# Kernel optimization log

Measured on AMD Instinct MI355X. Metric: run time of the kernel, lower is better.

The kernel has to match this reference:

```python
import jax, jax.numpy as jnp
import numpy as np

TAU = 2.0      # LIF membrane time constant
ALPHA = 4.0    # sigmoid surrogate sharpness (spikingjelly default)
EPS = 1e-5     # BatchNorm eps
HEADS = 8


def lif(x, vth):
    """MultiStepLIFNode: scan over leading time dim T. Hard reset to 0, detach_reset.
    Forward spike = heaviside(h - vth); backward uses sigmoid surrogate via straight-through."""
    def step(v, xt):
        h = v + (xt - v) / TAU
        hv = h - vth
        sg = jax.nn.sigmoid(ALPHA * hv)
        hard = (hv >= 0).astype(h.dtype)
        spike = sg + jax.lax.stop_gradient(hard - sg)
        v_new = h * (1.0 - jax.lax.stop_gradient(spike))  # detach_reset=True, v_reset=0
        return v_new, spike
    _, spikes = jax.lax.scan(step, jnp.zeros_like(x[0]), x)
    return spikes


def bn(x, gamma, beta, mean, var):
    # x: (T,B,C,N), params: (C,) ; eval-mode BatchNorm1d over channel axis 2
    inv = (gamma * jax.lax.rsqrt(var + EPS))[None, None, :, None]
    return (x - mean[None, None, :, None]) * inv + beta[None, None, :, None]


def setup_inputs() -> dict:
    key = jax.random.key(0)
    T, B, C, H, W = 4, 16, 384, 32, 32
    ks = jax.random.split(key, 24)
    d = {"x": jax.random.normal(ks[0], (T, B, C, H, W), jnp.float32)}
    i = 1
    wscale = 1.0 / np.sqrt(C)
    for p in ("q", "k", "v", "p"):
        d[p + "_w"] = jax.random.normal(ks[i], (C, C), jnp.float32) * wscale; i += 1
        d[p + "_gamma"] = jax.random.uniform(ks[i], (C,), jnp.float32, 0.5, 1.5); i += 1
        d[p + "_beta"] = jax.random.normal(ks[i], (C,), jnp.float32) * 0.1; i += 1
        d[p + "_mean"] = jax.random.normal(ks[i], (C,), jnp.float32) * 0.1; i += 1
        d[p + "_var"] = jax.random.uniform(ks[i], (C,), jnp.float32, 0.5, 1.5); i += 1
    d["p_bias"] = jax.random.normal(ks[i], (C,), jnp.float32) * 0.1
    return d


def reference(x, q_w, q_gamma, q_beta, q_mean, q_var,
              k_w, k_gamma, k_beta, k_mean, k_var,
              v_w, v_gamma, v_beta, v_mean, v_var,
              p_w, p_bias, p_gamma, p_beta, p_mean, p_var):
    T, B, C, H, W = x.shape
    N = H * W
    Ch = C // HEADS
    # input spiking (named proj_lif in source, applied first)
    xs = lif(x, 1.0).reshape(T, B, C, N)

    def branch(w, g, b, m, v):
        y = jnp.einsum('tbcn,dc->tbdn', xs, w)  # 1x1 Conv1d == channel matmul
        return lif(bn(y, g, b, m, v), 1.0).reshape(T, B, HEADS, Ch, N)

    q = branch(q_w, q_gamma, q_beta, q_mean, q_var)
    k = branch(k_w, k_gamma, k_beta, k_mean, k_var)
    v = branch(v_w, v_gamma, v_beta, v_mean, v_var)

    attn = jnp.sum(k * v, axis=3, keepdims=True)  # (T,B,h,1,N)
    attn = lif(attn, 0.5)
    out = (q * attn).reshape(T, B, C, N)
    out = jnp.einsum('tbcn,dc->tbdn', out, p_w) + p_bias[None, None, :, None]
    out = bn(out, p_gamma, p_beta, p_mean, p_var)
    return out.reshape(T, B, C, H, W)
```

## Files before the change

kernel.cpp:

```cpp
#include <hip/hip_runtime.h>

typedef unsigned short u16;
typedef unsigned char u8;
typedef unsigned int u32;
typedef float f32x4 __attribute__((ext_vector_type(4)));
typedef __bf16 bf16x8 __attribute__((ext_vector_type(8)));

#define SPB 6291456

__device__ __forceinline__ void gll16(const void* g, void* l) {
  __builtin_amdgcn_global_load_lds((const __attribute__((address_space(1))) void*)g,
                                   (__attribute__((address_space(3))) void*)l, 16, 0, 0);
}

__device__ __forceinline__ uint4 expand8(uint2 v, u32 t) {
  u32 a = v.x >> t, b = v.y >> t;
  uint4 r;
  r.x = ((a & 1u) ? 0x3F80u : 0u) | ((a & 0x100u) ? 0x3F800000u : 0u);
  r.y = ((a & 0x10000u) ? 0x3F80u : 0u) | ((a & 0x1000000u) ? 0x3F800000u : 0u);
  r.z = ((b & 1u) ? 0x3F80u : 0u) | ((b & 0x100u) ? 0x3F800000u : 0u);
  r.w = ((b & 0x10000u) ? 0x3F80u : 0u) | ((b & 0x1000000u) ? 0x3F800000u : 0u);
  return r;
}

__global__ __launch_bounds__(256) void k_convert(
    const float* __restrict__ qw, const float* __restrict__ kw,
    const float* __restrict__ vw, const float* __restrict__ pw,
    const float* __restrict__ qg, const float* __restrict__ qbt,
    const float* __restrict__ qm, const float* __restrict__ qv,
    const float* __restrict__ kg, const float* __restrict__ kbt,
    const float* __restrict__ km, const float* __restrict__ kv,
    const float* __restrict__ vg, const float* __restrict__ vbt,
    const float* __restrict__ vm, const float* __restrict__ vv,
    const float* __restrict__ pg, const float* __restrict__ pbt,
    const float* __restrict__ pm, const float* __restrict__ pv,
    const float* __restrict__ pbias,
    u16* __restrict__ Wstk, u16* __restrict__ Pw,
    float4* __restrict__ BNP, float4* __restrict__ PP) {
  int tid = blockIdx.x * 256 + threadIdx.x;
  if (tid < 442368) {
    int r = tid / 384, c = tid - r * 384;
    const float* src = (r < 384) ? qw : (r < 768) ? kw : vw;
    int rr = (r >= 768) ? r - 768 : (r >= 384) ? r - 384 : r;
    unsigned int u = __float_as_uint(src[rr * 384 + c]);
    u = (u + 0x7FFFu + ((u >> 16) & 1u)) >> 16;
    Wstk[tid] = (u16)u;
  } else if (tid < 589824) {
    int i = tid - 442368;
    unsigned int u = __float_as_uint(pw[i]);
    u = (u + 0x7FFFu + ((u >> 16) & 1u)) >> 16;
    Pw[i] = (u16)u;
  } else if (tid < 590976) {
    int r = tid - 589824;
    int br = r / 384, ch = r - br * 384;
    const float* g  = (br == 0) ? qg  : (br == 1) ? kg  : vg;
    const float* bt = (br == 0) ? qbt : (br == 1) ? kbt : vbt;
    const float* m  = (br == 0) ? qm  : (br == 1) ? km  : vm;
    const float* va = (br == 0) ? qv  : (br == 1) ? kv  : vv;
    float inv = g[ch] / sqrtf(va[ch] + 1e-5f);
    BNP[r] = make_float4(inv, m[ch], bt[ch], 0.f);
  } else if (tid < 591360) {
    int ch = tid - 590976;
    float inv = pg[ch] / sqrtf(pv[ch] + 1e-5f);
    PP[ch] = make_float4(inv, pm[ch], pbt[ch], pbias[ch]);
  }
}

__global__ __launch_bounds__(256) void k_lif_in(const float* __restrict__ x, u8* __restrict__ xsb) {
  const int nt = blockIdx.x, ct = blockIdx.y, b = blockIdx.z;
  const int tid = threadIdx.x;
  const int nj = tid & 63, cr = tid >> 6;
  const int c0 = ct * 64, n0 = nt * 64;
  __shared__ u32 nibs[64 * 65];
  float v[16];
  u32 nib[16];
  #pragma unroll
  for (int i = 0; i < 16; ++i) { v[i] = 0.f; nib[i] = 0u; }
  for (int t = 0; t < 4; ++t) {
    const float* xr = x + (((t * 16 + b) * 384 + c0 + cr) * 1024) + n0 + nj;
    #pragma unroll
    for (int it = 0; it < 16; ++it) {
      float xv = xr[it * 4096];
      float vv = v[it];
      float h = __fadd_rn(vv, __fmul_rn(__fsub_rn(xv, vv), 0.5f));
      bool s = h >= 1.f;
      v[it] = s ? 0.f : h;
      nib[it] |= (s ? 1u : 0u) << t;
    }
  }
  #pragma unroll
  for (int it = 0; it < 16; ++it) nibs[nj * 65 + cr + it * 4] = nib[it];
  __syncthreads();
  const int n = tid >> 2, ch = tid & 3;
  u32 w0[4];
  #pragma unroll
  for (int q = 0; q < 4; ++q) {
    u32 acc = 0;
    #pragma unroll
    for (int i = 0; i < 4; ++i)
      acc |= (nibs[n * 65 + ch * 16 + q * 4 + i] & 0xFu) << (8 * i);
    w0[q] = acc;
  }
  *(uint4*)(xsb + ((size_t)(b * 1024 + n0 + n)) * 384 + c0 + ch * 16) =
      make_uint4(w0[0], w0[1], w0[2], w0[3]);
}

#define GISSUE(kt) do { \
    gll16(Wp + (kt) * 32, &lds[((kt) % 3) * 12288 + wst]); \
    xr0[(kt) % 3] = *(const uint2*)(Xb0 + (kt) * 32); \
    xr1[(kt) % 3] = *(const uint2*)(Xb1 + (kt) * 32); \
  } while (0)

#define GWRITE(kt) do { \
    *(uint4*)&lds[((kt) % 3) * 12288 + 4096 + wst + lx8] = expand8(xr0[(kt) % 3], t_row); \
    *(uint4*)&lds[((kt) % 3) * 12288 + 8192 + wst + lx8] = expand8(xr1[(kt) % 3], t_row); \
  } while (0)

#define COMPUTE(bufi) do { \
    const u16* lb_ = &lds[(bufi) * 12288]; \
    bf16x8 ax[4], bw[4]; \
    _Pragma("unroll") \
    for (int ji = 0; ji < 4; ++ji) \
      ax[ji] = *(const bf16x8*)&lb_[4096 + (wjg * 64 + ji * 16 + l15) * 32 + swoff]; \
    _Pragma("unroll") \
    for (int ci = 0; ci < 4; ++ci) \
      bw[ci] = *(const bf16x8*)&lb_[(wcg * 64 + ci * 16 + l15) * 32 + swoff]; \
    __builtin_amdgcn_s_setprio(1); \
    _Pragma("unroll") \
    for (int ji = 0; ji < 4; ++ji) \
      _Pragma("unroll") \
      for (int ci = 0; ci < 4; ++ci) \
        acc[ji][ci] = __builtin_amdgcn_mfma_f32_16x16x32_bf16(ax[ji], bw[ci], acc[ji][ci], 0, 0, 0); \
    __builtin_amdgcn_s_setprio(0); \
  } while (0)

#define GSTEP(kt, VN, ISS) do { \
    asm volatile("s_waitcnt vmcnt(" #VN ")" ::: "memory"); \
    GWRITE(kt); \
    asm volatile("s_waitcnt lgkmcnt(0)" ::: "memory"); \
    __builtin_amdgcn_s_barrier(); \
    asm volatile("" ::: "memory"); \
    ISS; \
    COMPUTE((kt) % 3); \
  } while (0)

#define GEMM_PIPELINE() do { \
    GISSUE(0); GISSUE(1); \
    GSTEP(0, 3, GISSUE(2)); \
    GSTEP(1, 3, GISSUE(3)); \
    GSTEP(2, 3, GISSUE(4)); \
    GSTEP(3, 3, GISSUE(5)); \
    GSTEP(4, 3, GISSUE(6)); \
    GSTEP(5, 3, GISSUE(7)); \
    GSTEP(6, 3, GISSUE(8)); \
    GSTEP(7, 3, GISSUE(9)); \
    GSTEP(8, 3, GISSUE(10)); \
    GSTEP(9, 3, GISSUE(11)); \
    GSTEP(10, 3, ); \
    GSTEP(11, 0, ); \
  } while (0)

#define GEMM_SETUP(WSRC, XSRC) \
  const int tid = threadIdx.x; \
  const int w = tid >> 6, l = tid & 63; \
  const int wjg = w >> 1, wcg = w & 1; \
  const int l15 = tid & 15; \
  const int swoff = (((tid & 63) >> 4) ^ ((l15 >> 1) & 3)) * 8; \
  const int m0 = mt * 128; \
  const int wst = w * 512; \
  const int lx8 = l * 8; \
  const int row = w * 16 + (l >> 2); \
  const u32 t_row = (u32)(row & 3); \
  const int sch = (l & 3) ^ ((l >> 3) & 3); \
  const u16* Wp = (WSRC) + (m0 + row) * 384 + sch * 8; \
  const u8* Xb0 = (XSRC) + ((size_t)(b * 1024 + jt * 64 + (row >> 2))) * 384 + sch * 8; \
  const u8* Xb1 = Xb0 + 32 * 384; \
  uint2 xr0[3], xr1[3]; \
  f32x4 acc[4][4]; \
  const f32x4 zero = {0.f, 0.f, 0.f, 0.f}; \
  _Pragma("unroll") \
  for (int ji = 0; ji < 4; ++ji) \
    _Pragma("unroll") \
    for (int ci = 0; ci < 4; ++ci) acc[ji][ci] = zero;

__global__ __launch_bounds__(512, 4) void k_qkv(
    const u16* __restrict__ Wstk, const u8* __restrict__ xsb,
    const float4* __restrict__ BNP, u8* __restrict__ sp) {
  const int jt = blockIdx.x, mt = blockIdx.y, b = blockIdx.z;
  __shared__ u16 lds[36864];
  __shared__ float4 PRM[128];
  if (threadIdx.x < 128) PRM[threadIdx.x] = BNP[mt * 128 + threadIdx.x];
  __syncthreads();

  GEMM_SETUP(Wstk, xsb);
  GEMM_PIPELINE();

  const int br = mt / 3;
  const int cb = (mt - br * 3) * 128;
  const int g = (tid & 63) >> 4;
  u8* spW = sp + (size_t)br * SPB;
  #pragma unroll
  for (int ci = 0; ci < 4; ++ci) {
    const int c_loc = wcg * 64 + ci * 16 + l15;
    float4 pr = PRM[c_loc];
    #pragma unroll
    for (int ji = 0; ji < 4; ++ji) {
      f32x4 a = acc[ji][ci];
      u32 bits = 0;
      float v = 0.f;
      #pragma unroll
      for (int t = 0; t < 4; ++t) {
        float z = __fadd_rn(__fmul_rn(__fsub_rn(a[t], pr.y), pr.x), pr.z);
        float h = __fadd_rn(v, __fmul_rn(__fsub_rn(z, v), 0.5f));
        bool s = h >= 1.f;
        v = s ? 0.f : h;
        bits |= (s ? 1u : 0u) << t;
      }
      const int n_comb = b * 1024 + jt * 64 + wjg * 16 + ji * 4 + g;
      spW[(size_t)n_comb * 384 + cb + c_loc] = (u8)bits;
    }
  }
}

__global__ __launch_bounds__(256) void k_attn(const u8* __restrict__ sp, u8* __restrict__ xpb) {
  const int gw = blockIdx.x * 4 + (threadIdx.x >> 6);
  const int l = threadIdx.x & 63;
  const int b = gw >> 10, n = gw & 1023;
  const u8* qB = sp;
  const u8* kB = sp + SPB;
  const u8* vB = sp + 2 * SPB;
  const int base = (b * 1024 + n) * 384 + l * 6;
  u16 qu[3], ku[3], vu[3];
  #pragma unroll
  for (int i = 0; i < 3; ++i) {
    qu[i] = *(const u16*)(qB + base + 2 * i);
    ku[i] = *(const u16*)(kB + base + 2 * i);
    vu[i] = *(const u16*)(vB + base + 2 * i);
  }
  u32 s = 0;
  #pragma unroll
  for (int i = 0; i < 3; ++i) {
    u32 a = (u32)(ku[i] & vu[i]);
    #pragma unroll
    for (int t = 0; t < 4; ++t) {
      u32 x = (a >> t) & 0x0101u;
      s += ((x + (x >> 8)) & 3u) << (8 * t);
    }
  }
  s += __shfl_xor(s, 1);
  s += __shfl_xor(s, 2);
  s += __shfl_xor(s, 4);
  float v = 0.f;
  u32 m8 = 0;
  #pragma unroll
  for (int t = 0; t < 4; ++t) {
    float attn = (float)((s >> (8 * t)) & 0xFFu);
    float h = __fadd_rn(v, __fmul_rn(__fsub_rn(attn, v), 0.5f));
    bool sk = h >= 0.5f;
    v = sk ? 0.f : h;
    m8 |= (sk ? 1u : 0u) << t;
  }
  const u16 mm = (u16)(m8 * 0x0101u);
  u16* dst = (u16*)(xpb + base);
  #pragma unroll
  for (int i = 0; i < 3; ++i) dst[i] = qu[i] & mm;
}

__global__ __launch_bounds__(512, 4) void k_proj(
    const u16* __restrict__ Pw, const u8* __restrict__ xpb,
    const float4* __restrict__ PP, float* __restrict__ out) {
  const int jt = blockIdx.x, mt = blockIdx.y, b = blockIdx.z;
  __shared__ u16 lds[36864];
  __shared__ float4 PRM[128];
  if (threadIdx.x < 128) PRM[threadIdx.x] = PP[mt * 128 + threadIdx.x];
  __syncthreads();

  GEMM_SETUP(Pw, xpb);
  GEMM_PIPELINE();

  __syncthreads();
  float* scr = (float*)lds;
  const int n0im = jt * 64;
  const int g = (tid & 63) >> 4;

  #pragma unroll
  for (int t = 0; t < 4; ++t) {
    #pragma unroll
    for (int ci = 0; ci < 4; ++ci) {
      const int c_loc = wcg * 64 + ci * 16 + l15;
      float4 pr = PRM[c_loc];
      #pragma unroll
      for (int ji = 0; ji < 4; ++ji) {
        const int n_loc = wjg * 16 + ji * 4 + g;
        float zz = __fadd_rn(acc[ji][ci][t], pr.w);
        zz = __fadd_rn(__fmul_rn(__fsub_rn(zz, pr.y), pr.x), pr.z);
        scr[c_loc * 68 + n_loc] = zz;
      }
    }
    __syncthreads();
    #pragma unroll
    for (int it = 0; it < 4; ++it) {
      int slot = tid + it * 512;
      int c = slot >> 4, li = slot & 15;
      float4 val = *(const float4*)&scr[c * 68 + li * 4];
      *(float4*)&out[(((size_t)(t * 16 + b) * 384) + mt * 128 + c) * 1024 + n0im + li * 4] = val;
    }
    __syncthreads();
  }
}

extern "C" void kernel_launch(void* const* d_in, const int* in_sizes, int n_in,
                              void* d_out, int out_size, void* d_ws, size_t ws_size,
                              hipStream_t stream) {
  (void)in_sizes; (void)n_in; (void)out_size; (void)ws_size;
  const float* x   = (const float*)d_in[0];
  const float* qw  = (const float*)d_in[1];
  const float* qg  = (const float*)d_in[2];
  const float* qbt = (const float*)d_in[3];
  const float* qm  = (const float*)d_in[4];
  const float* qv  = (const float*)d_in[5];
  const float* kw  = (const float*)d_in[6];
  const float* kg  = (const float*)d_in[7];
  const float* kbt = (const float*)d_in[8];
  const float* km  = (const float*)d_in[9];
  const float* kv  = (const float*)d_in[10];
  const float* vw  = (const float*)d_in[11];
  const float* vg  = (const float*)d_in[12];
  const float* vbt = (const float*)d_in[13];
  const float* vm  = (const float*)d_in[14];
  const float* vv  = (const float*)d_in[15];
  const float* pw  = (const float*)d_in[16];
  const float* pg  = (const float*)d_in[17];
  const float* pbt = (const float*)d_in[18];
  const float* pm  = (const float*)d_in[19];
  const float* pv  = (const float*)d_in[20];
  const float* pbias = (const float*)d_in[21];

  char* ws = (char*)d_ws;
  u8*  xsb   = (u8*)ws;
  u8*  sp    = (u8*)(ws + 6291456);
  u8*  xpb   = (u8*)(ws + 25165824);
  u16* Wstk  = (u16*)(ws + 31457280);
  u16* Pw    = (u16*)(ws + 32342016);
  float4* BNP = (float4*)(ws + 32636928);
  float4* PP  = (float4*)(ws + 32655360);

  k_convert<<<2310, 256, 0, stream>>>(qw, kw, vw, pw, qg, qbt, qm, qv, kg, kbt, km, kv,
                                      vg, vbt, vm, vv, pg, pbt, pm, pv, pbias,
                                      Wstk, Pw, BNP, PP);
  k_lif_in<<<dim3(16, 6, 16), 256, 0, stream>>>(x, xsb);
  k_qkv<<<dim3(16, 9, 16), 512, 0, stream>>>(Wstk, xsb, BNP, sp);
  k_attn<<<4096, 256, 0, stream>>>(sp, xpb);
  k_proj<<<dim3(16, 3, 16), 512, 0, stream>>>(Pw, xpb, PP, (float*)d_out);
}
```

Measured before the change: 130.3 us.

## Compute three weight tiles per block to reuse expanded spike tiles in GEMMs

Each GEMM block now loads and expands its spike activation tile once, then multiplies it against three 128-row weight tiles (the q/k/v branches in qkv, all three output-channel slices in proj) with three accumulator sets. This cuts redundant activation loads and bit-to-bf16 expansion, and the grids shrink by a factor of three. The spike expansion also switches to byte-permute and multiply instead of per-bit selects. In exchange, register use and LDS per block grow (occupancy hint drops from 4 to 2), and proj now launches only 256 blocks, which may underfill the GPU.

```diff
diff --git a/kernel.cpp b/kernel.cpp
--- a/kernel.cpp
+++ b/kernel.cpp
@@ -13,13 +13,14 @@
                                    (__attribute__((address_space(3))) void*)l, 16, 0, 0);
 }
 
-__device__ __forceinline__ uint4 expand8(uint2 v, u32 t) {
-  u32 a = v.x >> t, b = v.y >> t;
+__device__ __forceinline__ uint4 expand8f(uint2 v, u32 t) {
+  u32 a = (v.x >> t) & 0x01010101u;
+  u32 b = (v.y >> t) & 0x01010101u;
   uint4 r;
-  r.x = ((a & 1u) ? 0x3F80u : 0u) | ((a & 0x100u) ? 0x3F800000u : 0u);
-  r.y = ((a & 0x10000u) ? 0x3F80u : 0u) | ((a & 0x1000000u) ? 0x3F800000u : 0u);
-  r.z = ((b & 1u) ? 0x3F80u : 0u) | ((b & 0x100u) ? 0x3F800000u : 0u);
-  r.w = ((b & 0x10000u) ? 0x3F80u : 0u) | ((b & 0x1000000u) ? 0x3F800000u : 0u);
+  r.x = __builtin_amdgcn_perm(0u, a, 0x0C010C00u) * 0x3F80u;
+  r.y = __builtin_amdgcn_perm(0u, a, 0x0C030C02u) * 0x3F80u;
+  r.z = __builtin_amdgcn_perm(0u, b, 0x0C010C00u) * 0x3F80u;
+  r.w = __builtin_amdgcn_perm(0u, b, 0x0C030C02u) * 0x3F80u;
   return r;
 }
 
@@ -105,121 +106,135 @@
       make_uint4(w0[0], w0[1], w0[2], w0[3]);
 }
 
+#define BUFU16 20480
+
 #define GISSUE(kt) do { \
-    gll16(Wp + (kt) * 32, &lds[((kt) % 3) * 12288 + wst]); \
+    u16* wb_ = &lds[((kt) % 3) * BUFU16 + wst]; \
+    gll16(Wp0 + (kt) * 32, wb_); \
+    gll16(Wp1 + (kt) * 32, wb_ + 4096); \
+    gll16(Wp2 + (kt) * 32, wb_ + 8192); \
     xr0[(kt) % 3] = *(const uint2*)(Xb0 + (kt) * 32); \
     xr1[(kt) % 3] = *(const uint2*)(Xb1 + (kt) * 32); \
   } while (0)
 
 #define GWRITE(kt) do { \
-    *(uint4*)&lds[((kt) % 3) * 12288 + 4096 + wst + lx8] = expand8(xr0[(kt) % 3], t_row); \
-    *(uint4*)&lds[((kt) % 3) * 12288 + 8192 + wst + lx8] = expand8(xr1[(kt) % 3], t_row); \
-  } while (0)
-
-#define COMPUTE(bufi) do { \
-    const u16* lb_ = &lds[(bufi) * 12288]; \
-    bf16x8 ax[4], bw[4]; \
+    *(uint4*)&lds[((kt) % 3) * BUFU16 + 12288 + tid * 8] = expand8f(xr0[(kt) % 3], t_row); \
+    *(uint4*)&lds[((kt) % 3) * BUFU16 + 12288 + 4096 + tid * 8] = expand8f(xr1[(kt) % 3], t_row); \
+  } while (0)
+
+#define MFMA4(accA, p) do { \
+    _Pragma("unroll") \
+    for (int ci = 0; ci < 4; ++ci) { \
+      bf16x8 bw_ = *(const bf16x8*)&lb_[(p) * 4096 + (wcg * 64 + ci * 16 + l15) * 32 + swoff]; \
+      _Pragma("unroll") \
+      for (int ji = 0; ji < 4; ++ji) \
+        accA[ji][ci] = __builtin_amdgcn_mfma_f32_16x16x32_bf16(ax[ji], bw_, accA[ji][ci], 0, 0, 0); \
+    } \
+  } while (0)
+
+#define COMPUTE3(bufi) do { \
+    const u16* lb_ = &lds[(bufi) * BUFU16]; \
+    bf16x8 ax[4]; \
     _Pragma("unroll") \
     for (int ji = 0; ji < 4; ++ji) \
-      ax[ji] = *(const bf16x8*)&lb_[4096 + (wjg * 64 + ji * 16 + l15) * 32 + swoff]; \
-    _Pragma("unroll") \
-    for (int ci = 0; ci < 4; ++ci) \
-      bw[ci] = *(const bf16x8*)&lb_[(wcg * 64 + ci * 16 + l15) * 32 + swoff]; \
+      ax[ji] = *(const bf16x8*)&lb_[12288 + (wjg * 64 + ji * 16 + l15) * 32 + swoff]; \
     __builtin_amdgcn_s_setprio(1); \
-    _Pragma("unroll") \
-    for (int ji = 0; ji < 4; ++ji) \
-      _Pragma("unroll") \
-      for (int ci = 0; ci < 4; ++ci) \
-        acc[ji][ci] = __builtin_amdgcn_mfma_f32_16x16x32_bf16(ax[ji], bw[ci], acc[ji][ci], 0, 0, 0); \
+    MFMA4(acc0, 0); MFMA4(acc1, 1); MFMA4(acc2, 2); \
     __builtin_amdgcn_s_setprio(0); \
   } while (0)
 
-#define GSTEP(kt, VN, ISS) do { \
+#define GSTEP(t, VN, TAIL) do { \
     asm volatile("s_waitcnt vmcnt(" #VN ")" ::: "memory"); \
-    GWRITE(kt); \
+    GWRITE(t); \
     asm volatile("s_waitcnt lgkmcnt(0)" ::: "memory"); \
     __builtin_amdgcn_s_barrier(); \
     asm volatile("" ::: "memory"); \
-    ISS; \
-    COMPUTE((kt) % 3); \
-  } while (0)
-
-#define GEMM_PIPELINE() do { \
+    TAIL; \
+    COMPUTE3((t) % 3); \
+  } while (0)
+
+#define GEMM_PIPELINE3() do { \
     GISSUE(0); GISSUE(1); \
-    GSTEP(0, 3, GISSUE(2)); \
-    GSTEP(1, 3, GISSUE(3)); \
-    GSTEP(2, 3, GISSUE(4)); \
-    GSTEP(3, 3, GISSUE(5)); \
-    GSTEP(4, 3, GISSUE(6)); \
-    GSTEP(5, 3, GISSUE(7)); \
-    GSTEP(6, 3, GISSUE(8)); \
-    GSTEP(7, 3, GISSUE(9)); \
-    GSTEP(8, 3, GISSUE(10)); \
-    GSTEP(9, 3, GISSUE(11)); \
-    GSTEP(10, 3, ); \
+    GSTEP(0, 5, GISSUE(2)); \
+    GSTEP(1, 5, GISSUE(3)); \
+    GSTEP(2, 5, GISSUE(4)); \
+    GSTEP(3, 5, GISSUE(5)); \
+    GSTEP(4, 5, GISSUE(6)); \
+    GSTEP(5, 5, GISSUE(7)); \
+    GSTEP(6, 5, GISSUE(8)); \
+    GSTEP(7, 5, GISSUE(9)); \
+    GSTEP(8, 5, GISSUE(10)); \
+    GSTEP(9, 5, GISSUE(11)); \
+    GSTEP(10, 5, ); \
     GSTEP(11, 0, ); \
   } while (0)
 
-#define GEMM_SETUP(WSRC, XSRC) \
+#define GEMM_SETUP() \
   const int tid = threadIdx.x; \
   const int w = tid >> 6, l = tid & 63; \
   const int wjg = w >> 1, wcg = w & 1; \
-  const int l15 = tid & 15; \
-  const int swoff = (((tid & 63) >> 4) ^ ((l15 >> 1) & 3)) * 8; \
-  const int m0 = mt * 128; \
+  const int l15 = tid & 15, g = l >> 4; \
+  const int swoff = (g ^ ((l15 >> 1) & 3)) * 8; \
   const int wst = w * 512; \
-  const int lx8 = l * 8; \
-  const int row = w * 16 + (l >> 2); \
+  const int row = tid >> 2; \
   const u32 t_row = (u32)(row & 3); \
   const int sch = (l & 3) ^ ((l >> 3) & 3); \
-  const u16* Wp = (WSRC) + (m0 + row) * 384 + sch * 8; \
-  const u8* Xb0 = (XSRC) + ((size_t)(b * 1024 + jt * 64 + (row >> 2))) * 384 + sch * 8; \
-  const u8* Xb1 = Xb0 + 32 * 384; \
   uint2 xr0[3], xr1[3]; \
-  f32x4 acc[4][4]; \
-  const f32x4 zero = {0.f, 0.f, 0.f, 0.f}; \
-  _Pragma("unroll") \
-  for (int ji = 0; ji < 4; ++ji) \
-    _Pragma("unroll") \
-    for (int ci = 0; ci < 4; ++ci) acc[ji][ci] = zero;
-
-__global__ __launch_bounds__(512, 4) void k_qkv(
+  f32x4 acc0[4][4], acc1[4][4], acc2[4][4]; \
+  { const f32x4 zero_ = {0.f, 0.f, 0.f, 0.f}; \
+    _Pragma("unroll") \
+    for (int ji = 0; ji < 4; ++ji) \
+      _Pragma("unroll") \
+      for (int ci = 0; ci < 4; ++ci) { acc0[ji][ci] = zero_; acc1[ji][ci] = zero_; acc2[ji][ci] = zero_; } }
+
+__global__ __launch_bounds__(512, 2) void k_qkv(
     const u16* __restrict__ Wstk, const u8* __restrict__ xsb,
     const float4* __restrict__ BNP, u8* __restrict__ sp) {
-  const int jt = blockIdx.x, mt = blockIdx.y, b = blockIdx.z;
-  __shared__ u16 lds[36864];
-  __shared__ float4 PRM[128];
-  if (threadIdx.x < 128) PRM[threadIdx.x] = BNP[mt * 128 + threadIdx.x];
-  __syncthreads();
-
-  GEMM_SETUP(Wstk, xsb);
-  GEMM_PIPELINE();
-
-  const int br = mt / 3;
-  const int cb = (mt - br * 3) * 128;
-  const int g = (tid & 63) >> 4;
-  u8* spW = sp + (size_t)br * SPB;
-  #pragma unroll
-  for (int ci = 0; ci < 4; ++ci) {
-    const int c_loc = wcg * 64 + ci * 16 + l15;
-    float4 pr = PRM[c_loc];
-    #pragma unroll
-    for (int ji = 0; ji < 4; ++ji) {
-      f32x4 a = acc[ji][ci];
-      u32 bits = 0;
-      float v = 0.f;
-      #pragma unroll
-      for (int t = 0; t < 4; ++t) {
-        float z = __fadd_rn(__fmul_rn(__fsub_rn(a[t], pr.y), pr.x), pr.z);
-        float h = __fadd_rn(v, __fmul_rn(__fsub_rn(z, v), 0.5f));
-        bool s = h >= 1.f;
-        v = s ? 0.f : h;
-        bits |= (s ? 1u : 0u) << t;
-      }
-      const int n_comb = b * 1024 + jt * 64 + wjg * 16 + ji * 4 + g;
-      spW[(size_t)n_comb * 384 + cb + c_loc] = (u8)bits;
-    }
-  }
+  const int jt = blockIdx.x, cb = blockIdx.y, b = blockIdx.z;
+  __shared__ u16 lds[61440];
+  __shared__ float4 PRM[384];
+
+  GEMM_SETUP();
+
+  if (tid < 384) PRM[tid] = BNP[(tid >> 7) * 384 + cb * 128 + (tid & 127)];
+  asm volatile("s_waitcnt vmcnt(0)" ::: "memory");
+
+  const u16* Wp0 = Wstk + (size_t)(cb * 128 + row) * 384 + sch * 8;
+  const u16* Wp1 = Wp0 + 147456;
+  const u16* Wp2 = Wp1 + 147456;
+  const u8* Xb0 = xsb + ((size_t)(b * 1024 + jt * 64 + (row >> 2))) * 384 + sch * 8;
+  const u8* Xb1 = Xb0 + 32 * 384;
+
+  GEMM_PIPELINE3();
+
+  const int n_base = b * 1024 + jt * 64 + wjg * 16 + g;
+#define QKV_EPI(accA, br) do { \
+    u8* spW = sp + (size_t)(br) * SPB; \
+    _Pragma("unroll") \
+    for (int ci = 0; ci < 4; ++ci) { \
+      const int c_loc = wcg * 64 + ci * 16 + l15; \
+      float4 pr = PRM[(br) * 128 + c_loc]; \
+      _Pragma("unroll") \
+      for (int ji = 0; ji < 4; ++ji) { \
+        f32x4 a = accA[ji][ci]; \
+        u32 bits = 0; \
+        float vv = 0.f; \
+        _Pragma("unroll") \
+        for (int t = 0; t < 4; ++t) { \
+          float z = __fadd_rn(__fmul_rn(__fsub_rn(a[t], pr.y), pr.x), pr.z); \
+          float h = __fadd_rn(vv, __fmul_rn(__fsub_rn(z, vv), 0.5f)); \
+          bool s = h >= 1.f; \
+          vv = s ? 0.f : h; \
+          bits |= (s ? 1u : 0u) << t; \
+        } \
+        spW[(size_t)(n_base + ji * 4) * 384 + cb * 128 + c_loc] = (u8)bits; \
+      } \
+    } \
+  } while (0)
+  QKV_EPI(acc0, 0);
+  QKV_EPI(acc1, 1);
+  QKV_EPI(acc2, 2);
+#undef QKV_EPI
 }
 
 __global__ __launch_bounds__(256) void k_attn(const u8* __restrict__ sp, u8* __restrict__ xpb) {
@@ -266,47 +281,58 @@
   for (int i = 0; i < 3; ++i) dst[i] = qu[i] & mm;
 }
 
-__global__ __launch_bounds__(512, 4) void k_proj(
+__global__ __launch_bounds__(512, 2) void k_proj(
     const u16* __restrict__ Pw, const u8* __restrict__ xpb,
     const float4* __restrict__ PP, float* __restrict__ out) {
-  const int jt = blockIdx.x, mt = blockIdx.y, b = blockIdx.z;
-  __shared__ u16 lds[36864];
-  __shared__ float4 PRM[128];
-  if (threadIdx.x < 128) PRM[threadIdx.x] = PP[mt * 128 + threadIdx.x];
-  __syncthreads();
-
-  GEMM_SETUP(Pw, xpb);
-  GEMM_PIPELINE();
+  const int jt = blockIdx.x, b = blockIdx.z;
+  __shared__ u16 lds[61440];
+  __shared__ float4 PRM[384];
+
+  GEMM_SETUP();
+
+  if (tid < 384) PRM[tid] = PP[tid];
+  asm volatile("s_waitcnt vmcnt(0)" ::: "memory");
+
+  const u16* Wp0 = Pw + (size_t)row * 384 + sch * 8;
+  const u16* Wp1 = Wp0 + 49152;
+  const u16* Wp2 = Wp1 + 49152;
+  const u8* Xb0 = xpb + ((size_t)(b * 1024 + jt * 64 + (row >> 2))) * 384 + sch * 8;
+  const u8* Xb1 = Xb0 + 32 * 384;
+
+  GEMM_PIPELINE3();
 
   __syncthreads();
   float* scr = (float*)lds;
   const int n0im = jt * 64;
-  const int g = (tid & 63) >> 4;
-
-  #pragma unroll
-  for (int t = 0; t < 4; ++t) {
-    #pragma unroll
-    for (int ci = 0; ci < 4; ++ci) {
-      const int c_loc = wcg * 64 + ci * 16 + l15;
-      float4 pr = PRM[c_loc];
-      #pragma unroll
-      for (int ji = 0; ji < 4; ++ji) {
-        const int n_loc = wjg * 16 + ji * 4 + g;
-        float zz = __fadd_rn(acc[ji][ci][t], pr.w);
-        zz = __fadd_rn(__fmul_rn(__fsub_rn(zz, pr.y), pr.x), pr.z);
-        scr[c_loc * 68 + n_loc] = zz;
-      }
-    }
-    __syncthreads();
-    #pragma unroll
-    for (int it = 0; it < 4; ++it) {
-      int slot = tid + it * 512;
-      int c = slot >> 4, li = slot & 15;
-      float4 val = *(const float4*)&scr[c * 68 + li * 4];
-      *(float4*)&out[(((size_t)(t * 16 + b) * 384) + mt * 128 + c) * 1024 + n0im + li * 4] = val;
-    }
-    __syncthreads();
-  }
+#define PROJ_EPI(accA, p) \
+  _Pragma("unroll") \
+  for (int t = 0; t < 4; ++t) { \
+    _Pragma("unroll") \
+    for (int ci = 0; ci < 4; ++ci) { \
+      const int c_loc = wcg * 64 + ci * 16 + l15; \
+      float4 pr = PRM[(p) * 128 + c_loc]; \
+      _Pragma("unroll") \
+      for (int ji = 0; ji < 4; ++ji) { \
+        const int n_loc = wjg * 16 + ji * 4 + g; \
+        float zz = __fadd_rn(accA[ji][ci][t], pr.w); \
+        zz = __fadd_rn(__fmul_rn(__fsub_rn(zz, pr.y), pr.x), pr.z); \
+        scr[c_loc * 68 + n_loc] = zz; \
+      } \
+    } \
+    __syncthreads(); \
+    _Pragma("unroll") \
+    for (int it = 0; it < 4; ++it) { \
+      int slot = tid + it * 512; \
+      int c = slot >> 4, li = slot & 15; \
+      float4 val = *(const float4*)&scr[c * 68 + li * 4]; \
+      *(float4*)&out[(((size_t)(t * 16 + b) * 384) + (p) * 128 + c) * 1024 + n0im + li * 4] = val; \
+    } \
+    __syncthreads(); \
+  }
+  PROJ_EPI(acc0, 0)
+  PROJ_EPI(acc1, 1)
+  PROJ_EPI(acc2, 2)
+#undef PROJ_EPI
 }
 
 extern "C" void kernel_launch(void* const* d_in, const int* in_sizes, int n_in,
@@ -349,7 +375,7 @@
                                       vg, vbt, vm, vv, pg, pbt, pm, pv, pbias,
                                       Wstk, Pw, BNP, PP);
   k_lif_in<<<dim3(16, 6, 16), 256, 0, stream>>>(x, xsb);
-  k_qkv<<<dim3(16, 9, 16), 512, 0, stream>>>(Wstk, xsb, BNP, sp);
+  k_qkv<<<dim3(16, 3, 16), 512, 0, stream>>>(Wstk, xsb, BNP, sp);
   k_attn<<<4096, 256, 0, stream>>>(sp, xpb);
-  k_proj<<<dim3(16, 3, 16), 512, 0, stream>>>(Pw, xpb, PP, (float*)d_out);
-}
+  k_proj<<<dim3(16, 1, 16), 512, 0, stream>>>(Pw, xpb, PP, (float*)d_out);
+}
```

After: 171.9 us. 31.9% more time.

## Stage packed spike tile in LDS once and deepen weight pipeline to six slots

Applied to the files above, without the earlier changes.

Each GEMM block now copies its whole packed-spike activation tile (64 positions by 384 channels) into LDS up front. It expands the spike bits to bf16 per k-step straight from LDS, using byte-permute plus multiply instead of per-bit selects. Weight tiles are loaded with a six-slot global-to-LDS ring, five k-steps ahead. This drops the per-step VGPR staging and LDS write-back of expanded activations and the lgkmcnt wait. BN parameters are read from global instead of LDS. The risk is more ALU work in the inner loop, since every wave re-expands its activations each step, and a larger LDS footprint that may reduce occupancy.

```diff
diff --git a/kernel.cpp b/kernel.cpp
--- a/kernel.cpp
+++ b/kernel.cpp
@@ -13,13 +13,14 @@
                                    (__attribute__((address_space(3))) void*)l, 16, 0, 0);
 }
 
-__device__ __forceinline__ uint4 expand8(uint2 v, u32 t) {
-  u32 a = v.x >> t, b = v.y >> t;
+__device__ __forceinline__ uint4 expand8f(uint2 v, u32 t) {
+  u32 a = (v.x >> t) & 0x01010101u;
+  u32 b = (v.y >> t) & 0x01010101u;
   uint4 r;
-  r.x = ((a & 1u) ? 0x3F80u : 0u) | ((a & 0x100u) ? 0x3F800000u : 0u);
-  r.y = ((a & 0x10000u) ? 0x3F80u : 0u) | ((a & 0x1000000u) ? 0x3F800000u : 0u);
-  r.z = ((b & 1u) ? 0x3F80u : 0u) | ((b & 0x100u) ? 0x3F800000u : 0u);
-  r.w = ((b & 0x10000u) ? 0x3F80u : 0u) | ((b & 0x1000000u) ? 0x3F800000u : 0u);
+  r.x = __builtin_amdgcn_perm(0u, a, 0x0C010C00u) * 0x3F80u;
+  r.y = __builtin_amdgcn_perm(0u, a, 0x0C030C02u) * 0x3F80u;
+  r.z = __builtin_amdgcn_perm(0u, b, 0x0C010C00u) * 0x3F80u;
+  r.w = __builtin_amdgcn_perm(0u, b, 0x0C030C02u) * 0x3F80u;
   return r;
 }
 
@@ -105,119 +106,118 @@
       make_uint4(w0[0], w0[1], w0[2], w0[3]);
 }
 
-#define GISSUE(kt) do { \
-    gll16(Wp + (kt) * 32, &lds[((kt) % 3) * 12288 + wst]); \
-    xr0[(kt) % 3] = *(const uint2*)(Xb0 + (kt) * 32); \
-    xr1[(kt) % 3] = *(const uint2*)(Xb1 + (kt) * 32); \
+#define XLDS_U16 13312
+#define WSLOT_U16 4096
+
+#define GISSUE(kt) gll16(Wp + (kt) * 32, &lds[XLDS_U16 + ((kt) % 6) * WSLOT_U16 + wst])
+
+#define SYNCP(n) do { \
+    asm volatile("s_waitcnt vmcnt(" #n ")" ::: "memory"); \
+    __builtin_amdgcn_s_barrier(); \
+    asm volatile("" ::: "memory"); \
   } while (0)
 
-#define GWRITE(kt) do { \
-    *(uint4*)&lds[((kt) % 3) * 12288 + 4096 + wst + lx8] = expand8(xr0[(kt) % 3], t_row); \
-    *(uint4*)&lds[((kt) % 3) * 12288 + 8192 + wst + lx8] = expand8(xr1[(kt) % 3], t_row); \
+#define COMPUTE(kt) do { \
+    const u8* xb_ = (const u8*)lds; \
+    const u16* wb_ = &lds[XLDS_U16 + ((kt) % 6) * WSLOT_U16]; \
+    bf16x8 ax[4]; \
+    _Pragma("unroll") \
+    for (int ji = 0; ji < 4; ++ji) { \
+      uint2 xr_ = *(const uint2*)(xb_ + (wjg * 16 + ji * 4 + d4) * 416 + (kt) * 32 + g8); \
+      uint4 e_ = expand8f(xr_, t_lane); \
+      ax[ji] = *(bf16x8*)&e_; \
+    } \
+    __builtin_amdgcn_s_setprio(1); \
+    _Pragma("unroll") \
+    for (int ci = 0; ci < 4; ++ci) { \
+      bf16x8 bw_ = *(const bf16x8*)&wb_[(wcg * 64 + ci * 16 + l15) * 32 + swoff]; \
+      _Pragma("unroll") \
+      for (int ji = 0; ji < 4; ++ji) \
+        acc[ji][ci] = __builtin_amdgcn_mfma_f32_16x16x32_bf16(ax[ji], bw_, acc[ji][ci], 0, 0, 0); \
+    } \
+    __builtin_amdgcn_s_setprio(0); \
   } while (0)
 
-#define COMPUTE(bufi) do { \
-    const u16* lb_ = &lds[(bufi) * 12288]; \
-    bf16x8 ax[4], bw[4]; \
-    _Pragma("unroll") \
-    for (int ji = 0; ji < 4; ++ji) \
-      ax[ji] = *(const bf16x8*)&lb_[4096 + (wjg * 64 + ji * 16 + l15) * 32 + swoff]; \
-    _Pragma("unroll") \
-    for (int ci = 0; ci < 4; ++ci) \
-      bw[ci] = *(const bf16x8*)&lb_[(wcg * 64 + ci * 16 + l15) * 32 + swoff]; \
-    __builtin_amdgcn_s_setprio(1); \
+#define GEMM_PIPELINE() do { \
+    GISSUE(0); GISSUE(1); GISSUE(2); GISSUE(3); GISSUE(4); \
+    SYNCP(4); GISSUE(5);  COMPUTE(0); \
+    SYNCP(4); GISSUE(6);  COMPUTE(1); \
+    SYNCP(4); GISSUE(7);  COMPUTE(2); \
+    SYNCP(4); GISSUE(8);  COMPUTE(3); \
+    SYNCP(4); GISSUE(9);  COMPUTE(4); \
+    SYNCP(4); GISSUE(10); COMPUTE(5); \
+    SYNCP(4); GISSUE(11); COMPUTE(6); \
+    SYNCP(4); COMPUTE(7); \
+    SYNCP(3); COMPUTE(8); \
+    SYNCP(2); COMPUTE(9); \
+    SYNCP(1); COMPUTE(10); \
+    SYNCP(0); COMPUTE(11); \
+  } while (0)
+
+#define XSTAGE(XSRC) do { \
+    const int xn_ = tid >> 3, xcp_ = tid & 7; \
+    const u8* xs_ = (XSRC) + (size_t)(b * 1024 + jt * 64 + xn_) * 384 + xcp_ * 48; \
+    u8* xd_ = (u8*)lds + xn_ * 416 + xcp_ * 48; \
+    uint4 v0_ = *(const uint4*)(xs_); \
+    uint4 v1_ = *(const uint4*)(xs_ + 16); \
+    uint4 v2_ = *(const uint4*)(xs_ + 32); \
+    *(uint4*)(xd_) = v0_; *(uint4*)(xd_ + 16) = v1_; *(uint4*)(xd_ + 32) = v2_; \
+    __syncthreads(); \
+  } while (0)
+
+#define GEMM_SETUP() \
+  const int tid = threadIdx.x; \
+  const int w = tid >> 6, l = tid & 63; \
+  const int wjg = w >> 1, wcg = w & 1; \
+  const int l15 = tid & 15, g = l >> 4; \
+  const int swoff = (g ^ ((l15 >> 1) & 3)) * 8; \
+  const int wst = w * 512; \
+  const int d4 = l15 >> 2, g8 = g * 8; \
+  const u32 t_lane = (u32)(l15 & 3); \
+  const int sch = (l & 3) ^ ((l >> 3) & 3); \
+  f32x4 acc[4][4]; \
+  { const f32x4 zero_ = {0.f, 0.f, 0.f, 0.f}; \
     _Pragma("unroll") \
     for (int ji = 0; ji < 4; ++ji) \
       _Pragma("unroll") \
-      for (int ci = 0; ci < 4; ++ci) \
-        acc[ji][ci] = __builtin_amdgcn_mfma_f32_16x16x32_bf16(ax[ji], bw[ci], acc[ji][ci], 0, 0, 0); \
-    __builtin_amdgcn_s_setprio(0); \
-  } while (0)
-
-#define GSTEP(kt, VN, ISS) do { \
-    asm volatile("s_waitcnt vmcnt(" #VN ")" ::: "memory"); \
-    GWRITE(kt); \
-    asm volatile("s_waitcnt lgkmcnt(0)" ::: "memory"); \
-    __builtin_amdgcn_s_barrier(); \
-    asm volatile("" ::: "memory"); \
-    ISS; \
-    COMPUTE((kt) % 3); \
-  } while (0)
-
-#define GEMM_PIPELINE() do { \
-    GISSUE(0); GISSUE(1); \
-    GSTEP(0, 3, GISSUE(2)); \
-    GSTEP(1, 3, GISSUE(3)); \
-    GSTEP(2, 3, GISSUE(4)); \
-    GSTEP(3, 3, GISSUE(5)); \
-    GSTEP(4, 3, GISSUE(6)); \
-    GSTEP(5, 3, GISSUE(7)); \
-    GSTEP(6, 3, GISSUE(8)); \
-    GSTEP(7, 3, GISSUE(9)); \
-    GSTEP(8, 3, GISSUE(10)); \
-    GSTEP(9, 3, GISSUE(11)); \
-    GSTEP(10, 3, ); \
-    GSTEP(11, 0, ); \
-  } while (0)
-
-#define GEMM_SETUP(WSRC, XSRC) \
-  const int tid = threadIdx.x; \
-  const int w = tid >> 6, l = tid & 63; \
-  const int wjg = w >> 1, wcg = w & 1; \
-  const int l15 = tid & 15; \
-  const int swoff = (((tid & 63) >> 4) ^ ((l15 >> 1) & 3)) * 8; \
-  const int m0 = mt * 128; \
-  const int wst = w * 512; \
-  const int lx8 = l * 8; \
-  const int row = w * 16 + (l >> 2); \
-  const u32 t_row = (u32)(row & 3); \
-  const int sch = (l & 3) ^ ((l >> 3) & 3); \
-  const u16* Wp = (WSRC) + (m0 + row) * 384 + sch * 8; \
-  const u8* Xb0 = (XSRC) + ((size_t)(b * 1024 + jt * 64 + (row >> 2))) * 384 + sch * 8; \
-  const u8* Xb1 = Xb0 + 32 * 384; \
-  uint2 xr0[3], xr1[3]; \
-  f32x4 acc[4][4]; \
-  const f32x4 zero = {0.f, 0.f, 0.f, 0.f}; \
-  _Pragma("unroll") \
-  for (int ji = 0; ji < 4; ++ji) \
-    _Pragma("unroll") \
-    for (int ci = 0; ci < 4; ++ci) acc[ji][ci] = zero;
+      for (int ci = 0; ci < 4; ++ci) acc[ji][ci] = zero_; }
 
 __global__ __launch_bounds__(512, 4) void k_qkv(
     const u16* __restrict__ Wstk, const u8* __restrict__ xsb,
     const float4* __restrict__ BNP, u8* __restrict__ sp) {
   const int jt = blockIdx.x, mt = blockIdx.y, b = blockIdx.z;
-  __shared__ u16 lds[36864];
-  __shared__ float4 PRM[128];
-  if (threadIdx.x < 128) PRM[threadIdx.x] = BNP[mt * 128 + threadIdx.x];
-  __syncthreads();
-
-  GEMM_SETUP(Wstk, xsb);
+  __shared__ u16 lds[37888];
+
+  GEMM_SETUP();
+  XSTAGE(xsb);
+
+  const int m0 = mt * 128;
+  const u16* Wp = Wstk + (size_t)(m0 + w * 16 + (l >> 2)) * 384 + sch * 8;
+
   GEMM_PIPELINE();
 
   const int br = mt / 3;
   const int cb = (mt - br * 3) * 128;
-  const int g = (tid & 63) >> 4;
+  const int n_base = b * 1024 + jt * 64 + wjg * 16 + g;
   u8* spW = sp + (size_t)br * SPB;
   #pragma unroll
   for (int ci = 0; ci < 4; ++ci) {
     const int c_loc = wcg * 64 + ci * 16 + l15;
-    float4 pr = PRM[c_loc];
+    float4 pr = BNP[br * 384 + cb + c_loc];
     #pragma unroll
     for (int ji = 0; ji < 4; ++ji) {
       f32x4 a = acc[ji][ci];
       u32 bits = 0;
-      float v = 0.f;
+      float vv = 0.f;
       #pragma unroll
       for (int t = 0; t < 4; ++t) {
         float z = __fadd_rn(__fmul_rn(__fsub_rn(a[t], pr.y), pr.x), pr.z);
-        float h = __fadd_rn(v, __fmul_rn(__fsub_rn(z, v), 0.5f));
+        float h = __fadd_rn(vv, __fmul_rn(__fsub_rn(z, vv), 0.5f));
         bool s = h >= 1.f;
-        v = s ? 0.f : h;
+        vv = s ? 0.f : h;
         bits |= (s ? 1u : 0u) << t;
       }
-      const int n_comb = b * 1024 + jt * 64 + wjg * 16 + ji * 4 + g;
-      spW[(size_t)n_comb * 384 + cb + c_loc] = (u8)bits;
+      spW[(size_t)(n_base + ji * 4) * 384 + cb + c_loc] = (u8)bits;
     }
   }
 }
@@ -270,25 +270,29 @@
     const u16* __restrict__ Pw, const u8* __restrict__ xpb,
     const float4* __restrict__ PP, float* __restrict__ out) {
   const int jt = blockIdx.x, mt = blockIdx.y, b = blockIdx.z;
-  __shared__ u16 lds[36864];
-  __shared__ float4 PRM[128];
-  if (threadIdx.x < 128) PRM[threadIdx.x] = PP[mt * 128 + threadIdx.x];
-  __syncthreads();
-
-  GEMM_SETUP(Pw, xpb);
+  __shared__ u16 lds[37888];
+
+  GEMM_SETUP();
+  XSTAGE(xpb);
+
+  const int m0 = mt * 128;
+  const u16* Wp = Pw + (size_t)(m0 + w * 16 + (l >> 2)) * 384 + sch * 8;
+
   GEMM_PIPELINE();
 
   __syncthreads();
   float* scr = (float*)lds;
   const int n0im = jt * 64;
-  const int g = (tid & 63) >> 4;
+  float4 prc[4];
+  #pragma unroll
+  for (int ci = 0; ci < 4; ++ci) prc[ci] = PP[m0 + wcg * 64 + ci * 16 + l15];
 
   #pragma unroll
   for (int t = 0; t < 4; ++t) {
     #pragma unroll
     for (int ci = 0; ci < 4; ++ci) {
       const int c_loc = wcg * 64 + ci * 16 + l15;
-      float4 pr = PRM[c_loc];
+      float4 pr = prc[ci];
       #pragma unroll
       for (int ji = 0; ji < 4; ++ji) {
         const int n_loc = wjg * 16 + ji * 4 + g;
@@ -303,7 +307,7 @@
       int slot = tid + it * 512;
       int c = slot >> 4, li = slot & 15;
       float4 val = *(const float4*)&scr[c * 68 + li * 4];
-      *(float4*)&out[(((size_t)(t * 16 + b) * 384) + mt * 128 + c) * 1024 + n0im + li * 4] = val;
+      *(float4*)&out[(((size_t)(t * 16 + b) * 384) + m0 + c) * 1024 + n0im + li * 4] = val;
     }
     __syncthreads();
   }
```

New measurement: 123.1 us. -5.5%, faster.
